# Optimization experiments

Measured on AMD Instinct MI355X. Metric: run time of the kernel, lower is better.

Reference implementation:

```python
import jax, jax.numpy as jnp
import numpy as np
import math

VOCAB, D_MODEL, IN_DIM, OUT_DIM, BLOCK = 50257, 256, 64, 64, 2048

def setup_inputs() -> dict:
    key = jax.random.key(0)
    ks = jax.random.split(key, 8)
    B, S = 4, 1024
    x = jax.random.normal(ks[0], (B, S, IN_DIM), dtype=jnp.float32)
    embedding = jax.random.normal(ks[1], (VOCAB, D_MODEL), dtype=jnp.float32)
    wpe = 0.01 * jax.random.normal(ks[2], (BLOCK, D_MODEL), dtype=jnp.float32)
    lim_e = 1.0 / math.sqrt(IN_DIM)
    enc_w = jax.random.uniform(ks[3], (D_MODEL, IN_DIM), minval=-lim_e, maxval=lim_e, dtype=jnp.float32)
    enc_b = jax.random.uniform(ks[4], (D_MODEL,), minval=-lim_e, maxval=lim_e, dtype=jnp.float32)
    ln_g = jnp.ones((D_MODEL,), dtype=jnp.float32)
    ln_b = jnp.zeros((D_MODEL,), dtype=jnp.float32)
    lim_d = 1.0 / math.sqrt(D_MODEL)
    dec_w = jax.random.uniform(ks[5], (OUT_DIM, D_MODEL), minval=-lim_d, maxval=lim_d, dtype=jnp.float32)
    dec_b = jax.random.uniform(ks[6], (OUT_DIM,), minval=-lim_d, maxval=lim_d, dtype=jnp.float32)
    return {"x": x, "embedding": embedding, "wpe": wpe, "enc_w": enc_w, "enc_b": enc_b,
            "ln_g": ln_g, "ln_b": ln_b, "dec_w": dec_w, "dec_b": dec_b}

def _layernorm(h, g, b, eps=1e-5):
    mu = jnp.mean(h, axis=-1, keepdims=True)
    var = jnp.var(h, axis=-1, keepdims=True)
    return (h - mu) * jax.lax.rsqrt(var + eps) * g + b

def reference(x, embedding, wpe, enc_w, enc_b, ln_g, ln_b, dec_w, dec_b):
    B, S, _ = x.shape
    pos_emb = wpe[:S]                                  # [S, D]
    h = jnp.einsum('bsi,di->bsd', x, enc_w) + enc_b    # encoder
    h = h + pos_emb
    h = _layernorm(h, ln_g, ln_b)
    logits = jnp.einsum('bsd,vd->bsv', h, embedding) / math.sqrt(D_MODEL)
    probs = jax.nn.softmax(logits, axis=-1)            # [B, S, V]
    quantize = jnp.einsum('bsv,vd->bsd', probs, embedding)
    out = jnp.einsum('bsd,od->bso', quantize, dec_w) + dec_b
    return (out, jnp.argmax(probs, axis=-1))
```

## Files before the change

### kernel.cpp

```cpp
#include <hip/hip_runtime.h>
#include <math.h>

#define VOCAB   50257
#define VP      50272
#define NVT     1571
#define DM      256
#define INDIM   64
#define OUTDIM  64
#define NROWS   4096
#define SEQ     1024
#define NSLICE  8
#define NTT     64
#define MARGIN  5e-3f
#define FLAGCAP 1024
#define EP      264
#define FOFF    4.0f

typedef _Float16 f16;
typedef _Float16 half8 __attribute__((ext_vector_type(8)));
typedef _Float16 half4v __attribute__((ext_vector_type(4)));
typedef float floatx4 __attribute__((ext_vector_type(4)));

static __device__ __forceinline__ unsigned ldsaddr(const void* p)
{
    return (unsigned)(unsigned long long)(__attribute__((address_space(3))) const void*)p;
}

template <int NT>
static __device__ __forceinline__ void tr_pair(unsigned a, half4v& t0, half4v& t1)
{
    asm volatile("ds_read_b64_tr_b16 %0, %2 offset:%3\n\t"
                 "ds_read_b64_tr_b16 %1, %2 offset:%4"
                 : "=v"(t0), "=v"(t1)
                 : "v"(a), "i"(NT * 128), "i"(NT * 128 + 2048));
}

__global__ __launch_bounds__(256) void encode_ln_kernel(
    const float* __restrict__ x, const float* __restrict__ enc_w,
    const float* __restrict__ enc_b, const float* __restrict__ wpe,
    const float* __restrict__ ln_g, const float* __restrict__ ln_b,
    float* __restrict__ hs_out, f16* __restrict__ q_hi, f16* __restrict__ q_lo,
    int* flagcnt, int write_q)
{
    const int row = blockIdx.x;
    const int s   = row & (SEQ - 1);
    const int d   = threadIdx.x;

    __shared__ float xs[INDIM];
    __shared__ float w1[4], w2[4];

    if (d < INDIM) xs[d] = x[(size_t)row * INDIM + d];
    __syncthreads();

    const float4* wrow = (const float4*)(enc_w + (size_t)d * INDIM);
    float dot = 0.f;
#pragma unroll
    for (int i = 0; i < INDIM / 4; ++i) {
        float4 w4 = wrow[i];
        dot += w4.x * xs[i * 4 + 0] + w4.y * xs[i * 4 + 1]
             + w4.z * xs[i * 4 + 2] + w4.w * xs[i * 4 + 3];
    }
    float h = dot + enc_b[d] + wpe[(size_t)s * DM + d];

    float v1 = h, v2 = h * h;
#pragma unroll
    for (int mask = 1; mask < 64; mask <<= 1) {
        v1 += __shfl_xor(v1, mask, 64);
        v2 += __shfl_xor(v2, mask, 64);
    }
    if ((d & 63) == 0) { w1[d >> 6] = v1; w2[d >> 6] = v2; }
    __syncthreads();
    float S1 = w1[0] + w1[1] + w1[2] + w1[3];
    float S2 = w2[0] + w2[1] + w2[2] + w2[3];
    float mu  = S1 * (1.f / DM);
    float var = S2 * (1.f / DM) - mu * mu;
    float rs  = rsqrtf(var + 1e-5f);
    float hn  = (h - mu) * rs * ln_g[d] + ln_b[d];
    float hsv = hn * 0.0625f;
    hs_out[(size_t)row * DM + d] = hsv;
    if (write_q) {
        f16 hi = (f16)hsv;
        q_hi[(size_t)row * DM + d] = hi;
        q_lo[(size_t)row * DM + d] = (f16)(hsv - (float)hi);
    }
    if (row == 0 && d == 0 && write_q) *flagcnt = 0;
}

__global__ __launch_bounds__(256) void prep_emb(
    const float* __restrict__ emb, f16* __restrict__ e_hi)
{
    const size_t i = ((size_t)blockIdx.x * 256 + threadIdx.x) * 8;
    if (i >= (size_t)VP * DM) return;
    const size_t v = i >> 8;
    half8 h;
    if (v < VOCAB) {
        const float* src = emb + i;
        float4 f0 = *(const float4*)(src);
        float4 f1 = *(const float4*)(src + 4);
        h[0]=(f16)f0.x; h[1]=(f16)f0.y; h[2]=(f16)f0.z; h[3]=(f16)f0.w;
        h[4]=(f16)f1.x; h[5]=(f16)f1.y; h[6]=(f16)f1.z; h[7]=(f16)f1.w;
    } else {
#pragma unroll
        for (int j = 0; j < 8; ++j) h[j] = (f16)0.f;
    }
    *(half8*)(e_hi + i) = h;
}

__global__ __launch_bounds__(256, 2) void fused_main(
    const f16* __restrict__ e_hi, const f16* __restrict__ q_hi,
    float* __restrict__ pO, float* __restrict__ pm1, float* __restrict__ pm2,
    float* __restrict__ pl, int* __restrict__ pi1)
{
    const int tid  = threadIdx.x;
    const int wave = tid >> 6;
    const int lane = tid & 63;
    const int m_   = lane & 15;
    const int quad = lane >> 4;
    const int slice = blockIdx.x & 7;
    const int tt    = blockIdx.x >> 3;

    __shared__ f16 ehi_s[2][32 * DM];
    __shared__ f16 plds[4][16][40];

    half8 qf[8];
    const f16* qb = q_hi + ((size_t)(tt * 64 + wave * 16 + m_)) * DM + quad * 8;
#pragma unroll
    for (int s = 0; s < 8; ++s) qf[s] = *(const half8*)(qb + s * 32);

    floatx4 O[16];
#pragma unroll
    for (int i = 0; i < 16; ++i) { O[i][0]=0.f; O[i][1]=0.f; O[i][2]=0.f; O[i][3]=0.f; }
    float t1 = -INFINITY, t2 = -INFINITY, lacc = 0.f;
    int   ti = 0;

    const int ntile = (NVT - slice + NSLICE - 1) / NSLICE;

    const int aoff = (m_ >> 2) * 1024 + (m_ & 3) * 16 + (quad >> 1) * 64 + (quad & 1) * 8;

    const unsigned trbase = ldsaddr(&ehi_s[0][0]) + (unsigned)(quad * 4096 + m_ * 2);

    const int ssv = (lane >> 1) & 3;
    const int ssd = ((lane >> 3) << 4) + ((lane & 1) << 3);

#define STAGE_TILE(BB, V0)                                                              \
    {                                                                                   \
        _Pragma("unroll")                                                               \
        for (int i_ = 0; i_ < 2; ++i_) {                                                \
            _Pragma("unroll")                                                           \
            for (int j_ = 0; j_ < 2; ++j_) {                                            \
                const int vblk_ = wave * 2 + i_;                                        \
                const f16* src_ = e_hi + (size_t)((V0) + vblk_ * 4 + ssv) * DM          \
                                  + j_ * 128 + ssd;                                     \
                f16* dst_ = &ehi_s[(BB)][vblk_ * 1024 + j_ * 512];                      \
                __builtin_amdgcn_global_load_lds(                                       \
                    (const __attribute__((address_space(1))) void*)src_,                \
                    (__attribute__((address_space(3))) void*)dst_, 16, 0, 0);           \
            }                                                                           \
        }                                                                               \
    }

    STAGE_TILE(0, slice * 32);
    __syncthreads();

    for (int it = 0; it < ntile; ++it) {
        const int b  = it & 1;
        const int v0 = (slice + it * NSLICE) * 32;
        const bool pre = (it + 1 < ntile);

        if (pre) STAGE_TILE(b ^ 1, v0 + NSLICE * 32);

        floatx4 sf0, sf1;
        sf0[0]=0.f; sf0[1]=0.f; sf0[2]=0.f; sf0[3]=0.f;
        sf1[0]=0.f; sf1[1]=0.f; sf1[2]=0.f; sf1[3]=0.f;
        const f16* ab = &ehi_s[b][aoff];
#pragma unroll
        for (int s = 0; s < 8; ++s) {
            half8 a0 = *(const half8*)(ab + s * 128);
            half8 a1 = *(const half8*)(ab + 4096 + s * 128);
            sf0 = __builtin_amdgcn_mfma_f32_16x16x32_f16(a0, qf[s], sf0, 0, 0, 0);
            sf1 = __builtin_amdgcn_mfma_f32_16x16x32_f16(a1, qf[s], sf1, 0, 0, 0);
        }
        if (v0 + 32 > VOCAB) {
#pragma unroll
            for (int r = 0; r < 4; ++r) {
                if (v0 + quad * 4 + r >= VOCAB)      sf0[r] = -INFINITY;
                if (v0 + 16 + quad * 4 + r >= VOCAB) sf1[r] = -INFINITY;
            }
        }

        float p0[4], p1[4];
#pragma unroll
        for (int r = 0; r < 4; ++r) {
            float sv = sf0[r]; int vg = v0 + quad * 4 + r;
            t2 = fmaxf(t2, fminf(t1, sv));
            ti = (sv > t1) ? vg : ti;
            t1 = fmaxf(t1, sv);
            float e = __expf(sv - FOFF);
            lacc += e; p0[r] = e;
        }
#pragma unroll
        for (int r = 0; r < 4; ++r) {
            float sv = sf1[r]; int vg = v0 + 16 + quad * 4 + r;
            t2 = fmaxf(t2, fminf(t1, sv));
            ti = (sv > t1) ? vg : ti;
            t1 = fmaxf(t1, sv);
            float e = __expf(sv - FOFF);
            lacc += e; p1[r] = e;
        }

        {
            half4v h0, h1;
#pragma unroll
            for (int r = 0; r < 4; ++r) { h0[r] = (f16)p0[r]; h1[r] = (f16)p1[r]; }
            *(half4v*)(&plds[wave][m_][quad * 4])      = h0;
            *(half4v*)(&plds[wave][m_][16 + quad * 4]) = h1;
        }
        __asm__ volatile("s_waitcnt lgkmcnt(0)" ::: "memory");
        half8 a2 = *(const half8*)(&plds[wave][m_][quad * 8]);

        const unsigned trb = trbase + (unsigned)(b * 16384);
        half4v u0[8], u1[8];

        __builtin_amdgcn_sched_barrier(0);
        tr_pair<0>(trb, u0[0], u1[0]);
        tr_pair<1>(trb, u0[1], u1[1]);
        tr_pair<2>(trb, u0[2], u1[2]);
        tr_pair<3>(trb, u0[3], u1[3]);
        tr_pair<4>(trb, u0[4], u1[4]);
        tr_pair<5>(trb, u0[5], u1[5]);
        tr_pair<6>(trb, u0[6], u1[6]);
        tr_pair<7>(trb, u0[7], u1[7]);
        __asm__ volatile("s_waitcnt lgkmcnt(0)" ::: "memory");
        __builtin_amdgcn_sched_barrier(0);
#pragma unroll
        for (int nt = 0; nt < 8; ++nt) {
            half8 b2 = __builtin_shufflevector(u0[nt], u1[nt], 0, 1, 2, 3, 4, 5, 6, 7);
            O[nt] = __builtin_amdgcn_mfma_f32_16x16x32_f16(a2, b2, O[nt], 0, 0, 0);
        }
        tr_pair<8>(trb,  u0[0], u1[0]);
        tr_pair<9>(trb,  u0[1], u1[1]);
        tr_pair<10>(trb, u0[2], u1[2]);
        tr_pair<11>(trb, u0[3], u1[3]);
        tr_pair<12>(trb, u0[4], u1[4]);
        tr_pair<13>(trb, u0[5], u1[5]);
        tr_pair<14>(trb, u0[6], u1[6]);
        tr_pair<15>(trb, u0[7], u1[7]);
        __asm__ volatile("s_waitcnt lgkmcnt(0)" ::: "memory");
        __builtin_amdgcn_sched_barrier(0);
#pragma unroll
        for (int nt = 8; nt < 16; ++nt) {
            half8 b2 = __builtin_shufflevector(u0[nt - 8], u1[nt - 8], 0, 1, 2, 3, 4, 5, 6, 7);
            O[nt] = __builtin_amdgcn_mfma_f32_16x16x32_f16(a2, b2, O[nt], 0, 0, 0);
        }

        __syncthreads();
    }
#undef STAGE_TILE

#pragma unroll
    for (int offc = 16; offc <= 32; offc += 16) {
        float o1 = __shfl_xor(t1, offc);
        float o2 = __shfl_xor(t2, offc);
        int   oi = __shfl_xor(ti, offc);
        float ol = __shfl_xor(lacc, offc);
        t2 = fmaxf(fmaxf(t2, o2), fminf(t1, o1));
        ti = (o1 > t1) ? oi : ti;
        t1 = fmaxf(t1, o1);
        lacc += ol;
    }

    const int trow0 = tt * 64 + wave * 16;
    float* ob = pO + ((size_t)slice * NROWS + trow0) * DM;
#pragma unroll
    for (int nt = 0; nt < 16; ++nt)
#pragma unroll
        for (int r = 0; r < 4; ++r)
            ob[(size_t)(quad * 4 + r) * DM + nt * 16 + m_] = O[nt][r];
    if (lane < 16) {
        const int idx = slice * NROWS + trow0 + lane;
        pm1[idx] = t1;
        pm2[idx] = t2;
        pl [idx] = lacc;
        pi1[idx] = ti;
    }
}

__global__ __launch_bounds__(256) void merge_decode(
    const float* __restrict__ pO, const float* __restrict__ pm1,
    const float* __restrict__ pm2, const float* __restrict__ pl,
    const int* __restrict__ pi1,
    const float* __restrict__ dec_w, const float* __restrict__ dec_b,
    float* __restrict__ out, float* __restrict__ amax_out,
    unsigned long long* __restrict__ amax64, int* flagcnt, int* flaglist,
    int* __restrict__ flbyte)
{
    const int tt  = blockIdx.x;
    const int tid = threadIdx.x;
    __shared__ float q_s[16][DM];
    __shared__ float lI[16];

    if (tid < 16) {
        const int row = tt * 16 + tid;
        float M = -INFINITY, M2 = -INFINITY; int win = 0;
        float lt = 0.f;
        for (int s = 0; s < NSLICE; ++s) {
            float v = pm1[s * NROWS + row];
            if (v > M) { M2 = M; M = v; win = s; }
            else M2 = fmaxf(M2, v);
            M2 = fmaxf(M2, pm2[s * NROWS + row]);
            lt += pl[s * NROWS + row];
        }
        amax_out[row] = (float)pi1[win * NROWS + row];
        amax64[row] = 0ull;
        int fl = (M - M2) < MARGIN;
        flbyte[row] = fl;
        if (fl) {
            int pos = atomicAdd(flagcnt, 1);
            if (pos < FLAGCAP) flaglist[pos] = row;
        }
        lI[tid] = 1.f / lt;
    }
    __syncthreads();
    {
        const int m = tid >> 4, d0 = (tid & 15) * 16;
        const int row = tt * 16 + m;
        float4 acc[4];
#pragma unroll
        for (int k = 0; k < 4; ++k) acc[k] = make_float4(0.f, 0.f, 0.f, 0.f);
        for (int s = 0; s < NSLICE; ++s) {
            const float4* pp = (const float4*)(pO + ((size_t)s * NROWS + row) * DM + d0);
#pragma unroll
            for (int k = 0; k < 4; ++k) {
                float4 v = pp[k];
                acc[k].x += v.x; acc[k].y += v.y;
                acc[k].z += v.z; acc[k].w += v.w;
            }
        }
        const float li = lI[m];
#pragma unroll
        for (int k = 0; k < 4; ++k) {
            acc[k].x *= li; acc[k].y *= li; acc[k].z *= li; acc[k].w *= li;
            *(float4*)&q_s[m][d0 + k * 4] = acc[k];
        }
    }
    __syncthreads();
    {
        const int o = tid & 63;
        const float4* wp = (const float4*)(dec_w + (size_t)o * DM);
#pragma unroll
        for (int k = 0; k < 4; ++k) {
            const int m = (tid >> 6) + k * 4;
            const float4* qp = (const float4*)&q_s[m][0];
            float acc = 0.f;
            for (int d4 = 0; d4 < DM / 4; ++d4) {
                float4 w = wp[d4], q = qp[d4];
                acc += w.x * q.x + w.y * q.y + w.z * q.z + w.w * q.w;
            }
            out[(size_t)(tt * 16 + m) * OUTDIM + o] = acc + dec_b[o];
        }
    }
}

__global__ __launch_bounds__(256) void gather_flagged(
    const f16* __restrict__ q_hi, const f16* __restrict__ q_lo,
    const int* __restrict__ flagcnt, const int* __restrict__ flaglist,
    f16* __restrict__ qg)
{
    int cnt = *flagcnt; if (cnt > FLAGCAP) cnt = FLAGCAP;
    const int j = blockIdx.x;
    if (j >= cnt) return;
    const int row = flaglist[j];
    const int t = threadIdx.x;
    qg[(size_t)j * 512 + t]       = q_hi[(size_t)row * DM + t];
    qg[(size_t)j * 512 + 256 + t] = q_lo[(size_t)row * DM + t];
}

__global__ __launch_bounds__(64) void recheck_rows(
    const float* __restrict__ emb, const f16* __restrict__ qg,
    const int* __restrict__ flagcnt, const int* __restrict__ flaglist,
    unsigned long long* __restrict__ amax64)
{
    int cnt = *flagcnt; if (cnt > FLAGCAP) cnt = FLAGCAP;
    if (cnt == 0) return;
    const int v0   = blockIdx.x * 32;
    const int lane = threadIdx.x;
    const int m_   = lane & 15;
    const int quad = lane >> 4;

    __shared__ f16 ehi[32][EP];
    __shared__ f16 elo[32][EP];

    for (int i = 0; i < 32; ++i) {
        const int v = v0 + i;
        float4 f = (v < VOCAB) ? *(const float4*)(emb + (size_t)v * DM + lane * 4)
                               : make_float4(0.f, 0.f, 0.f, 0.f);
        half4v hh, hl;
        hh[0]=(f16)f.x; hh[1]=(f16)f.y; hh[2]=(f16)f.z; hh[3]=(f16)f.w;
        hl[0]=(f16)(f.x-(float)hh[0]); hl[1]=(f16)(f.y-(float)hh[1]);
        hl[2]=(f16)(f.z-(float)hh[2]); hl[3]=(f16)(f.w-(float)hh[3]);
        *(half4v*)&ehi[i][lane * 4] = hh;
        *(half4v*)&elo[i][lane * 4] = hl;
    }
    __asm__ volatile("s_waitcnt lgkmcnt(0)" ::: "memory");

    for (int c0 = 0; c0 < cnt; c0 += 16) {
        const bool haveb = (c0 + m_) < cnt;
        const int fidx = haveb ? (c0 + m_) : 0;

        half8 bh[8], bl[8];
        const f16* qb = qg + (size_t)fidx * 512 + quad * 8;
#pragma unroll
        for (int s = 0; s < 8; ++s) {
            bh[s] = *(const half8*)(qb + s * 32);
            bl[s] = *(const half8*)(qb + 256 + s * 32);
        }

        floatx4 C0, C1;
        C0[0]=0.f; C0[1]=0.f; C0[2]=0.f; C0[3]=0.f;
        C1[0]=0.f; C1[1]=0.f; C1[2]=0.f; C1[3]=0.f;
#pragma unroll
        for (int s = 0; s < 8; ++s) {
            half8 ah0 = *(const half8*)&ehi[m_][quad * 8 + 32 * s];
            half8 al0 = *(const half8*)&elo[m_][quad * 8 + 32 * s];
            half8 ah1 = *(const half8*)&ehi[m_ + 16][quad * 8 + 32 * s];
            half8 al1 = *(const half8*)&elo[m_ + 16][quad * 8 + 32 * s];
            C0 = __builtin_amdgcn_mfma_f32_16x16x32_f16(ah0, bh[s], C0, 0, 0, 0);
            C0 = __builtin_amdgcn_mfma_f32_16x16x32_f16(ah0, bl[s], C0, 0, 0, 0);
            C0 = __builtin_amdgcn_mfma_f32_16x16x32_f16(al0, bh[s], C0, 0, 0, 0);
            C0 = __builtin_amdgcn_mfma_f32_16x16x32_f16(al0, bl[s], C0, 0, 0, 0);
            C1 = __builtin_amdgcn_mfma_f32_16x16x32_f16(ah1, bh[s], C1, 0, 0, 0);
            C1 = __builtin_amdgcn_mfma_f32_16x16x32_f16(ah1, bl[s], C1, 0, 0, 0);
            C1 = __builtin_amdgcn_mfma_f32_16x16x32_f16(al1, bh[s], C1, 0, 0, 0);
            C1 = __builtin_amdgcn_mfma_f32_16x16x32_f16(al1, bl[s], C1, 0, 0, 0);
        }

        float bv = -INFINITY; int bi = 0;
#pragma unroll
        for (int r = 0; r < 4; ++r) {
            int v = v0 + quad * 4 + r;
            float val = (v < VOCAB) ? C0[r] : -INFINITY;
            if (val > bv) { bv = val; bi = v; }
            int v2 = v + 16;
            float val2 = (v2 < VOCAB) ? C1[r] : -INFINITY;
            if (val2 > bv) { bv = val2; bi = v2; }
        }
#pragma unroll
        for (int offc = 16; offc <= 32; offc += 16) {
            float ov = __shfl_xor(bv, offc);
            int   oi = __shfl_xor(bi, offc);
            if (ov > bv || (ov == bv && oi < bi)) { bv = ov; bi = oi; }
        }
        if (quad == 0 && haveb) {
            unsigned u = __float_as_uint(bv);
            u = (u & 0x80000000u) ? ~u : (u | 0x80000000u);
            unsigned long long key =
                ((unsigned long long)u << 32) | (unsigned)(~bi);
            atomicMax(&amax64[flaglist[fidx]], key);
        }
    }
}

__global__ void finalize_amax(const int* __restrict__ flbyte,
                              const unsigned long long* __restrict__ amax64,
                              float* __restrict__ amax_out)
{
    int row = blockIdx.x * 256 + threadIdx.x;
    if (row >= NROWS) return;
    if (flbyte[row]) {
        unsigned long long u = amax64[row];
        if (u) {
            unsigned idx = ~(unsigned)(u & 0xffffffffu);
            amax_out[row] = (float)idx;
        }
    }
}

#define RPB 4
__global__ __launch_bounds__(256, 2) void fused_softmax_quant_kernel(
    const float* __restrict__ emb, const float* __restrict__ hs,
    const float* __restrict__ dec_w, const float* __restrict__ dec_b,
    float* __restrict__ out, float* __restrict__ amax_out)
{
    const int tid  = threadIdx.x;
    const int g    = tid >> 4;
    const int q    = tid & 15;
    const int row0 = blockIdx.x * RPB;

    __shared__ __align__(16) float q_lds[RPB][DM];
    __shared__ float sm[16][RPB], sl[16][RPB];
    __shared__ int   sam[16][RPB];
    __shared__ float sLf[RPB];

    for (int i = tid; i < RPB * DM; i += 256) (&q_lds[0][0])[i] = 0.f;

    float4 hsr[RPB][4];
#pragma unroll
    for (int r = 0; r < RPB; ++r)
#pragma unroll
        for (int o = 0; o < 4; ++o)
            hsr[r][o] = *(const float4*)(hs + (size_t)(row0 + r) * DM + o * 64 + q * 4);

    float m[RPB], l[RPB];
    int   am[RPB];
    float4 acc[RPB][4];
#pragma unroll
    for (int r = 0; r < RPB; ++r) {
        m[r] = -INFINITY; l[r] = 0.f; am[r] = 0;
#pragma unroll
        for (int o = 0; o < 4; ++o) acc[r][o] = make_float4(0.f, 0.f, 0.f, 0.f);
    }

    float ecur[16], enxt[16];
    {
        size_t b0 = (size_t)g * DM + q * 4;
#pragma unroll
        for (int o = 0; o < 4; ++o)
            *(float4*)(enxt + o * 4) = *(const float4*)(emb + b0 + o * 64);
    }

#pragma unroll 1
    for (int v = g; v < VOCAB; v += 16) {
#pragma unroll
        for (int j = 0; j < 16; ++j) ecur[j] = enxt[j];
        int vn = (v + 16 < VOCAB) ? v + 16 : v;
        size_t bn = (size_t)vn * DM + q * 4;
#pragma unroll
        for (int o = 0; o < 4; ++o)
            *(float4*)(enxt + o * 4) = *(const float4*)(emb + bn + o * 64);

        float part[RPB];
#pragma unroll
        for (int r = 0; r < RPB; ++r) {
            const float* hp = (const float*)&hsr[r][0];
            float t = 0.f;
#pragma unroll
            for (int j = 0; j < 16; ++j) t += ecur[j] * hp[j];
            part[r] = t;
        }
#pragma unroll
        for (int mask = 8; mask >= 1; mask >>= 1)
#pragma unroll
            for (int r = 0; r < RPB; ++r)
                part[r] += __shfl_xor(part[r], mask, 16);

#pragma unroll
        for (int r = 0; r < RPB; ++r) {
            float lg = part[r];
            float* ap = (float*)&acc[r][0];
            if (lg > m[r]) {
                float c = __expf(m[r] - lg);
                m[r] = lg; am[r] = v;
                l[r] = l[r] * c + 1.f;
#pragma unroll
                for (int j = 0; j < 16; ++j) ap[j] = ap[j] * c + ecur[j];
            } else {
                float p = __expf(lg - m[r]);
                l[r] += p;
#pragma unroll
                for (int j = 0; j < 16; ++j) ap[j] += p * ecur[j];
            }
        }
    }

    if (q == 0) {
#pragma unroll
        for (int r = 0; r < RPB; ++r) { sm[g][r] = m[r]; sl[g][r] = l[r]; sam[g][r] = am[r]; }
    }
    __syncthreads();

    float wgt[RPB], Lr[RPB];
    int   A[RPB];
#pragma unroll
    for (int r = 0; r < RPB; ++r) {
        float M = -INFINITY; int a = 0;
        for (int gg = 0; gg < 16; ++gg) {
            float mv = sm[gg][r];
            if (mv > M) { M = mv; a = sam[gg][r]; }
        }
        float L = 0.f;
        for (int gg = 0; gg < 16; ++gg) L += sl[gg][r] * __expf(sm[gg][r] - M);
        wgt[r] = __expf(m[r] - M);
        Lr[r] = L; A[r] = a;
    }

#pragma unroll
    for (int r = 0; r < RPB; ++r) {
        const float* ap = (const float*)&acc[r][0];
#pragma unroll
        for (int j = 0; j < 16; ++j) {
            float vs = ap[j] * wgt[r];
            vs += __shfl_xor(vs, 16, 64);
            vs += __shfl_xor(vs, 32, 64);
            if ((g & 3) == 0) {
                int o = j >> 2, c = j & 3;
                atomicAdd(&q_lds[r][o * 64 + q * 4 + c], vs);
            }
        }
    }
    if (tid == 0) {
#pragma unroll
        for (int r = 0; r < RPB; ++r) {
            sLf[r] = Lr[r];
            amax_out[row0 + r] = (float)A[r];
        }
    }
    __syncthreads();

    {
        const int r = tid >> 6, o = tid & 63;
        const float4* dwp = (const float4*)(dec_w + (size_t)o * DM);
        const float4* qp  = (const float4*)&q_lds[r][0];
        float s = 0.f;
#pragma unroll 8
        for (int d4 = 0; d4 < DM / 4; ++d4) {
            float4 wv = dwp[d4];
            float4 qv = qp[d4];
            s += wv.x * qv.x + wv.y * qv.y + wv.z * qv.z + wv.w * qv.w;
        }
        s = s / sLf[r] + dec_b[o];
        out[(size_t)(row0 + r) * OUTDIM + o] = s;
    }
}

extern "C" void kernel_launch(void* const* d_in, const int* in_sizes, int n_in,
                              void* d_out, int out_size, void* d_ws, size_t ws_size,
                              hipStream_t stream)
{
    const float* x     = (const float*)d_in[0];
    const float* emb   = (const float*)d_in[1];
    const float* wpe   = (const float*)d_in[2];
    const float* enc_w = (const float*)d_in[3];
    const float* enc_b = (const float*)d_in[4];
    const float* ln_g  = (const float*)d_in[5];
    const float* ln_b  = (const float*)d_in[6];
    const float* dec_w = (const float*)d_in[7];
    const float* dec_b = (const float*)d_in[8];

    float* out      = (float*)d_out;
    float* amax_out = out + (size_t)NROWS * OUTDIM;

    char* w = (char*)d_ws;
    size_t off = 0;
    float* hs = (float*)(w + off);          off += (size_t)NROWS * DM * 4;
    f16* q_hi = (f16*)(w + off);            off += (size_t)NROWS * DM * 2;
    f16* q_lo = (f16*)(w + off);            off += (size_t)NROWS * DM * 2;
    f16* e_hi = (f16*)(w + off);            off += (size_t)VP * DM * 2;
    float* pO = (float*)(w + off);          off += (size_t)NSLICE * NROWS * DM * 4;
    float* pm1 = (float*)(w + off);         off += (size_t)NSLICE * NROWS * 4;
    float* pm2 = (float*)(w + off);         off += (size_t)NSLICE * NROWS * 4;
    float* pl  = (float*)(w + off);         off += (size_t)NSLICE * NROWS * 4;
    int*   pi1 = (int*)(w + off);           off += (size_t)NSLICE * NROWS * 4;
    unsigned long long* amax64 = (unsigned long long*)(w + off); off += (size_t)NROWS * 8;
    int* flagcnt  = (int*)(w + off);        off += 256;
    int* flaglist = (int*)(w + off);        off += FLAGCAP * 4;
    int* flbyte   = (int*)(w + off);        off += (size_t)NROWS * 4;
    f16* qg       = (f16*)(w + off);        off += (size_t)FLAGCAP * 512 * 2;

    const bool full = (ws_size >= off);

    encode_ln_kernel<<<NROWS, 256, 0, stream>>>(x, enc_w, enc_b, wpe, ln_g, ln_b,
                                                hs, q_hi, q_lo, flagcnt, full ? 1 : 0);
    if (full) {
        prep_emb<<<((size_t)VP * DM) / (256 * 8), 256, 0, stream>>>(emb, e_hi);
        fused_main<<<NTT * NSLICE, 256, 0, stream>>>(e_hi, q_hi,
                                                     pO, pm1, pm2, pl, pi1);
        merge_decode<<<NROWS / 16, 256, 0, stream>>>(pO, pm1, pm2, pl, pi1, dec_w, dec_b,
                                                     out, amax_out, amax64, flagcnt,
                                                     flaglist, flbyte);
        gather_flagged<<<FLAGCAP, 256, 0, stream>>>(q_hi, q_lo, flagcnt, flaglist, qg);
        recheck_rows<<<NVT, 64, 0, stream>>>(emb, qg, flagcnt, flaglist, amax64);
        finalize_amax<<<(NROWS + 255) / 256, 256, 0, stream>>>(flbyte, amax64, amax_out);
    } else {
        fused_softmax_quant_kernel<<<NROWS / RPB, 256, 0, stream>>>(emb, hs, dec_w,
                                                                    dec_b, out, amax_out);
    }
}
```

Baseline: 545.6 us.

## Switch fused_main to 32x32 MFMA with 64-wide vocab tiles

Rewrites the main logits/softmax/PV kernel to use 32x32x16 MFMA instead of 16x16x32, with 64-vocab tiles per iteration, waves split across token and vocab halves. The prefetch of the next tile moves after a barrier. The per-row max, second max and sum statistics are merged through shared memory at the end. The aim is fewer LDS reads per FLOP and less instruction overhead, at the cost of more LDS, an extra barrier per tile and higher register pressure from four 16-wide accumulators plus 16 q fragments.

```diff
diff --git a/kernel.cpp b/kernel.cpp
--- a/kernel.cpp
+++ b/kernel.cpp
@@ -2,7 +2,8 @@
 #include <math.h>
 
 #define VOCAB   50257
-#define VP      50272
+#define VP64    50304
+#define NT64    786
 #define NVT     1571
 #define DM      256
 #define INDIM   64
@@ -20,19 +21,18 @@
 typedef _Float16 half8 __attribute__((ext_vector_type(8)));
 typedef _Float16 half4v __attribute__((ext_vector_type(4)));
 typedef float floatx4 __attribute__((ext_vector_type(4)));
+typedef float f32x16 __attribute__((ext_vector_type(16)));
 
 static __device__ __forceinline__ unsigned ldsaddr(const void* p)
 {
     return (unsigned)(unsigned long long)(__attribute__((address_space(3))) const void*)p;
 }
 
-template <int NT>
-static __device__ __forceinline__ void tr_pair(unsigned a, half4v& t0, half4v& t1)
-{
-    asm volatile("ds_read_b64_tr_b16 %0, %2 offset:%3\n\t"
-                 "ds_read_b64_tr_b16 %1, %2 offset:%4"
-                 : "=v"(t0), "=v"(t1)
-                 : "v"(a), "i"(NT * 128), "i"(NT * 128 + 2048));
+template <int IMM>
+static __device__ __forceinline__ void trrd(unsigned a, half4v& d)
+{
+    asm volatile("ds_read_b64_tr_b16 %0, %1 offset:%2"
+                 : "=v"(d) : "v"(a), "i"(IMM));
 }
 
 __global__ __launch_bounds__(256) void encode_ln_kernel(
@@ -90,7 +90,7 @@
     const float* __restrict__ emb, f16* __restrict__ e_hi)
 {
     const size_t i = ((size_t)blockIdx.x * 256 + threadIdx.x) * 8;
-    if (i >= (size_t)VP * DM) return;
+    if (i >= (size_t)VP64 * DM) return;
     const size_t v = i >> 8;
     half8 h;
     if (v < VOCAB) {
@@ -114,174 +114,212 @@
     const int tid  = threadIdx.x;
     const int wave = tid >> 6;
     const int lane = tid & 63;
-    const int m_   = lane & 15;
-    const int quad = lane >> 4;
+    const int l31  = lane & 31;
+    const int h    = lane >> 5;
+    const int thalf = wave & 1;
+    const int vhalf = wave >> 1;
     const int slice = blockIdx.x & 7;
     const int tt    = blockIdx.x >> 3;
 
-    __shared__ f16 ehi_s[2][32 * DM];
-    __shared__ f16 plds[4][16][40];
-
-    half8 qf[8];
-    const f16* qb = q_hi + ((size_t)(tt * 64 + wave * 16 + m_)) * DM + quad * 8;
-#pragma unroll
-    for (int s = 0; s < 8; ++s) qf[s] = *(const half8*)(qb + s * 32);
-
-    floatx4 O[16];
-#pragma unroll
-    for (int i = 0; i < 16; ++i) { O[i][0]=0.f; O[i][1]=0.f; O[i][2]=0.f; O[i][3]=0.f; }
-    float t1 = -INFINITY, t2 = -INFINITY, lacc = 0.f;
-    int   ti = 0;
-
-    const int ntile = (NVT - slice + NSLICE - 1) / NSLICE;
-
-    const int aoff = (m_ >> 2) * 1024 + (m_ & 3) * 16 + (quad >> 1) * 64 + (quad & 1) * 8;
-
-    const unsigned trbase = ldsaddr(&ehi_s[0][0]) + (unsigned)(quad * 4096 + m_ * 2);
-
-    const int ssv = (lane >> 1) & 3;
-    const int ssd = ((lane >> 3) << 4) + ((lane & 1) << 3);
-
-#define STAGE_TILE(BB, V0)                                                              \
-    {                                                                                   \
-        _Pragma("unroll")                                                               \
-        for (int i_ = 0; i_ < 2; ++i_) {                                                \
-            _Pragma("unroll")                                                           \
-            for (int j_ = 0; j_ < 2; ++j_) {                                            \
-                const int vblk_ = wave * 2 + i_;                                        \
-                const f16* src_ = e_hi + (size_t)((V0) + vblk_ * 4 + ssv) * DM          \
-                                  + j_ * 128 + ssd;                                     \
-                f16* dst_ = &ehi_s[(BB)][vblk_ * 1024 + j_ * 512];                      \
-                __builtin_amdgcn_global_load_lds(                                       \
-                    (const __attribute__((address_space(1))) void*)src_,                \
-                    (__attribute__((address_space(3))) void*)dst_, 16, 0, 0);           \
-            }                                                                           \
-        }                                                                               \
-    }
-
-    STAGE_TILE(0, slice * 32);
+    __shared__ f16 ehi_s[2][64 * DM];
+    __shared__ f16 plds[64][72];
+    __shared__ float mmrg[2][32][3];
+    __shared__ int   imrg[2][32];
+
+    half8 qf[16];
+    {
+        const f16* qb = q_hi + ((size_t)(tt * 64 + thalf * 32 + l31)) * DM + h * 8;
+#pragma unroll
+        for (int s = 0; s < 16; ++s) qf[s] = *(const half8*)(qb + s * 16);
+    }
+
+    f32x16 O0, O1, O2, O3;
+#pragma unroll
+    for (int i = 0; i < 16; ++i) { O0[i]=0.f; O1[i]=0.f; O2[i]=0.f; O3[i]=0.f; }
+    float t1a = -INFINITY, t2a = -INFINITY, la_a = 0.f;
+    float t1b = -INFINITY, t2b = -INFINITY, la_b = 0.f;
+    int tia = 0, tib = 0;
+
+    const int ntile = (NT64 - slice + NSLICE - 1) / NSLICE;
+
+    const int aoff = (vhalf * 8 + (l31 >> 2)) * 1024 + (l31 & 3) * 16 + h * 8;
+
+    const unsigned trbase = ldsaddr(&ehi_s[0][0]) +
+        (unsigned)(vhalf * 1024 + h * 4096 + ((lane >> 4) & 1) * 128 + (lane & 15) * 2);
+
+    const int lan3 = lane >> 3;
+    const int lv   = (lane & 7) >> 1;
+    const int ld8  = (lane & 1) * 8;
+
+#define STAGE_TILE(BB, V0)                                                   \
+    {                                                                        \
+        _Pragma("unroll")                                                    \
+        for (int c_ = 0; c_ < 8; ++c_) {                                     \
+            const int sub_ = wave * 64 + c_ * 8 + lan3;                      \
+            const int v4_ = sub_ >> 4, d16_ = sub_ & 15;                     \
+            const f16* src_ = e_hi + (size_t)((V0) + v4_ * 4 + lv) * DM      \
+                              + d16_ * 16 + ld8;                             \
+            f16* dst_ = &ehi_s[(BB)][wave * 4096 + c_ * 512];                \
+            __builtin_amdgcn_global_load_lds(                                \
+                (const __attribute__((address_space(1))) void*)src_,         \
+                (__attribute__((address_space(3))) void*)dst_, 16, 0, 0);    \
+        }                                                                    \
+    }
+
+#define G2STEP(DL, OV)                                                         \
+    {                                                                          \
+        half4v u00, u01, u10, u11, u20, u21, u30, u31;                         \
+        trrd<(DL)*256 +     0>(tb, u00);                                       \
+        trrd<(DL)*256 +  2048>(tb, u01);                                       \
+        trrd<(DL)*256 +  8192>(tb, u10);                                       \
+        trrd<(DL)*256 + 10240>(tb, u11);                                       \
+        trrd<(DL)*256 + 16384>(tb, u20);                                       \
+        trrd<(DL)*256 + 18432>(tb, u21);                                       \
+        trrd<(DL)*256 + 24576>(tb, u30);                                       \
+        trrd<(DL)*256 + 26624>(tb, u31);                                       \
+        __asm__ volatile("s_waitcnt lgkmcnt(0)" ::: "memory");                 \
+        __builtin_amdgcn_sched_barrier(0);                                     \
+        __builtin_amdgcn_s_setprio(1);                                         \
+        OV = __builtin_amdgcn_mfma_f32_32x32x16_f16(pa0,                       \
+                 __builtin_shufflevector(u00, u01, 0,1,2,3,4,5,6,7), OV,0,0,0);\
+        OV = __builtin_amdgcn_mfma_f32_32x32x16_f16(pa1,                       \
+                 __builtin_shufflevector(u10, u11, 0,1,2,3,4,5,6,7), OV,0,0,0);\
+        OV = __builtin_amdgcn_mfma_f32_32x32x16_f16(pa2,                       \
+                 __builtin_shufflevector(u20, u21, 0,1,2,3,4,5,6,7), OV,0,0,0);\
+        OV = __builtin_amdgcn_mfma_f32_32x32x16_f16(pa3,                       \
+                 __builtin_shufflevector(u30, u31, 0,1,2,3,4,5,6,7), OV,0,0,0);\
+        __builtin_amdgcn_s_setprio(0);                                         \
+    }
+
+    STAGE_TILE(0, slice * 64);
     __syncthreads();
 
     for (int it = 0; it < ntile; ++it) {
         const int b  = it & 1;
-        const int v0 = (slice + it * NSLICE) * 32;
+        const int v0 = (slice + it * NSLICE) * 64;
         const bool pre = (it + 1 < ntile);
 
-        if (pre) STAGE_TILE(b ^ 1, v0 + NSLICE * 32);
-
-        floatx4 sf0, sf1;
-        sf0[0]=0.f; sf0[1]=0.f; sf0[2]=0.f; sf0[3]=0.f;
-        sf1[0]=0.f; sf1[1]=0.f; sf1[2]=0.f; sf1[3]=0.f;
-        const f16* ab = &ehi_s[b][aoff];
-#pragma unroll
-        for (int s = 0; s < 8; ++s) {
-            half8 a0 = *(const half8*)(ab + s * 128);
-            half8 a1 = *(const half8*)(ab + 4096 + s * 128);
-            sf0 = __builtin_amdgcn_mfma_f32_16x16x32_f16(a0, qf[s], sf0, 0, 0, 0);
-            sf1 = __builtin_amdgcn_mfma_f32_16x16x32_f16(a1, qf[s], sf1, 0, 0, 0);
-        }
-        if (v0 + 32 > VOCAB) {
-#pragma unroll
-            for (int r = 0; r < 4; ++r) {
-                if (v0 + quad * 4 + r >= VOCAB)      sf0[r] = -INFINITY;
-                if (v0 + 16 + quad * 4 + r >= VOCAB) sf1[r] = -INFINITY;
+        f32x16 C;
+#pragma unroll
+        for (int i = 0; i < 16; ++i) C[i] = 0.f;
+        {
+            const f16* ab = &ehi_s[b][aoff];
+            __builtin_amdgcn_s_setprio(1);
+#pragma unroll
+            for (int s = 0; s < 16; ++s)
+                C = __builtin_amdgcn_mfma_f32_32x32x16_f16(
+                        *(const half8*)(ab + s * 64), qf[s], C, 0, 0, 0);
+            __builtin_amdgcn_s_setprio(0);
+        }
+
+        if (v0 + 64 > VOCAB) {
+#pragma unroll
+            for (int r = 0; r < 16; ++r) {
+                int v = v0 + vhalf * 32 + (r & 3) + 8 * (r >> 2) + 4 * h;
+                if (v >= VOCAB) C[r] = -INFINITY;
             }
         }
 
-        float p0[4], p1[4];
-#pragma unroll
-        for (int r = 0; r < 4; ++r) {
-            float sv = sf0[r]; int vg = v0 + quad * 4 + r;
-            t2 = fmaxf(t2, fminf(t1, sv));
-            ti = (sv > t1) ? vg : ti;
-            t1 = fmaxf(t1, sv);
-            float e = __expf(sv - FOFF);
-            lacc += e; p0[r] = e;
-        }
-#pragma unroll
-        for (int r = 0; r < 4; ++r) {
-            float sv = sf1[r]; int vg = v0 + 16 + quad * 4 + r;
-            t2 = fmaxf(t2, fminf(t1, sv));
-            ti = (sv > t1) ? vg : ti;
-            t1 = fmaxf(t1, sv);
-            float e = __expf(sv - FOFF);
-            lacc += e; p1[r] = e;
-        }
-
         {
-            half4v h0, h1;
-#pragma unroll
-            for (int r = 0; r < 4; ++r) { h0[r] = (f16)p0[r]; h1[r] = (f16)p1[r]; }
-            *(half4v*)(&plds[wave][m_][quad * 4])      = h0;
-            *(half4v*)(&plds[wave][m_][16 + quad * 4]) = h1;
-        }
-        __asm__ volatile("s_waitcnt lgkmcnt(0)" ::: "memory");
-        half8 a2 = *(const half8*)(&plds[wave][m_][quad * 8]);
-
-        const unsigned trb = trbase + (unsigned)(b * 16384);
-        half4v u0[8], u1[8];
-
-        __builtin_amdgcn_sched_barrier(0);
-        tr_pair<0>(trb, u0[0], u1[0]);
-        tr_pair<1>(trb, u0[1], u1[1]);
-        tr_pair<2>(trb, u0[2], u1[2]);
-        tr_pair<3>(trb, u0[3], u1[3]);
-        tr_pair<4>(trb, u0[4], u1[4]);
-        tr_pair<5>(trb, u0[5], u1[5]);
-        tr_pair<6>(trb, u0[6], u1[6]);
-        tr_pair<7>(trb, u0[7], u1[7]);
-        __asm__ volatile("s_waitcnt lgkmcnt(0)" ::: "memory");
-        __builtin_amdgcn_sched_barrier(0);
-#pragma unroll
-        for (int nt = 0; nt < 8; ++nt) {
-            half8 b2 = __builtin_shufflevector(u0[nt], u1[nt], 0, 1, 2, 3, 4, 5, 6, 7);
-            O[nt] = __builtin_amdgcn_mfma_f32_16x16x32_f16(a2, b2, O[nt], 0, 0, 0);
-        }
-        tr_pair<8>(trb,  u0[0], u1[0]);
-        tr_pair<9>(trb,  u0[1], u1[1]);
-        tr_pair<10>(trb, u0[2], u1[2]);
-        tr_pair<11>(trb, u0[3], u1[3]);
-        tr_pair<12>(trb, u0[4], u1[4]);
-        tr_pair<13>(trb, u0[5], u1[5]);
-        tr_pair<14>(trb, u0[6], u1[6]);
-        tr_pair<15>(trb, u0[7], u1[7]);
-        __asm__ volatile("s_waitcnt lgkmcnt(0)" ::: "memory");
-        __builtin_amdgcn_sched_barrier(0);
-#pragma unroll
-        for (int nt = 8; nt < 16; ++nt) {
-            half8 b2 = __builtin_shufflevector(u0[nt - 8], u1[nt - 8], 0, 1, 2, 3, 4, 5, 6, 7);
-            O[nt] = __builtin_amdgcn_mfma_f32_16x16x32_f16(a2, b2, O[nt], 0, 0, 0);
+            f16* prow = &plds[thalf * 32 + l31][vhalf * 32 + h * 4];
+#pragma unroll
+            for (int g2 = 0; g2 < 4; ++g2) {
+                half4v hv;
+#pragma unroll
+                for (int j = 0; j < 4; ++j) {
+                    float e = __expf(C[g2 * 4 + j] - FOFF);
+                    hv[j] = (f16)e;
+                    if (g2 < 2) la_a += e; else la_b += e;
+                }
+                *(half4v*)(prow + g2 * 8) = hv;
+            }
+        }
+#pragma unroll
+        for (int r = 0; r < 8; ++r) {
+            float sv = C[r];
+            int vg = v0 + vhalf * 32 + (r & 3) + 8 * (r >> 2) + 4 * h;
+            t2a = fmaxf(t2a, fminf(t1a, sv));
+            tia = (sv > t1a) ? vg : tia;
+            t1a = fmaxf(t1a, sv);
+        }
+#pragma unroll
+        for (int r = 8; r < 16; ++r) {
+            float sv = C[r];
+            int vg = v0 + vhalf * 32 + (r & 3) + 8 * (r >> 2) + 4 * h;
+            t2b = fmaxf(t2b, fminf(t1b, sv));
+            tib = (sv > t1b) ? vg : tib;
+            t1b = fmaxf(t1b, sv);
         }
 
         __syncthreads();
+
+        if (pre) STAGE_TILE(b ^ 1, v0 + NSLICE * 64);
+
+        {
+            const f16* pb = &plds[thalf * 32 + l31][h * 8];
+            half8 pa0 = *(const half8*)(pb);
+            half8 pa1 = *(const half8*)(pb + 16);
+            half8 pa2 = *(const half8*)(pb + 32);
+            half8 pa3 = *(const half8*)(pb + 48);
+            const unsigned tb = trbase + (unsigned)(b * 32768);
+            G2STEP(0, O0)
+            G2STEP(1, O1)
+            G2STEP(2, O2)
+            G2STEP(3, O3)
+        }
+
+        __syncthreads();
     }
 #undef STAGE_TILE
-
-#pragma unroll
-    for (int offc = 16; offc <= 32; offc += 16) {
-        float o1 = __shfl_xor(t1, offc);
-        float o2 = __shfl_xor(t2, offc);
-        int   oi = __shfl_xor(ti, offc);
-        float ol = __shfl_xor(lacc, offc);
-        t2 = fmaxf(fmaxf(t2, o2), fminf(t1, o1));
-        ti = (o1 > t1) ? oi : ti;
-        t1 = fmaxf(t1, o1);
-        lacc += ol;
-    }
-
-    const int trow0 = tt * 64 + wave * 16;
-    float* ob = pO + ((size_t)slice * NROWS + trow0) * DM;
-#pragma unroll
-    for (int nt = 0; nt < 16; ++nt)
-#pragma unroll
-        for (int r = 0; r < 4; ++r)
-            ob[(size_t)(quad * 4 + r) * DM + nt * 16 + m_] = O[nt][r];
-    if (lane < 16) {
-        const int idx = slice * NROWS + trow0 + lane;
-        pm1[idx] = t1;
-        pm2[idx] = t2;
-        pl [idx] = lacc;
-        pi1[idx] = ti;
+#undef G2STEP
+
+    {
+        float* ob = pO + ((size_t)slice * NROWS + tt * 64 + thalf * 32) * DM + vhalf * 128;
+#pragma unroll
+        for (int r = 0; r < 16; ++r) {
+            const size_t rb = (size_t)((r & 3) + 8 * (r >> 2) + 4 * h) * DM + l31;
+            ob[rb +  0] = O0[r];
+            ob[rb + 32] = O1[r];
+            ob[rb + 64] = O2[r];
+            ob[rb + 96] = O3[r];
+        }
+    }
+
+    float nt1 = fmaxf(t1a, t1b);
+    float nt2 = fmaxf(fminf(t1a, t1b), fmaxf(t2a, t2b));
+    int   nti = (t1b > t1a) ? tib : tia;
+    float nl  = la_a + la_b;
+    {
+        float o1 = __shfl_xor(nt1, 32);
+        float o2 = __shfl_xor(nt2, 32);
+        int   oi = __shfl_xor(nti, 32);
+        float ol = __shfl_xor(nl, 32);
+        nt2 = fmaxf(fminf(nt1, o1), fmaxf(nt2, o2));
+        nti = (o1 > nt1) ? oi : nti;
+        nt1 = fmaxf(nt1, o1);
+        nl += ol;
+    }
+    if (vhalf == 1 && h == 0) {
+        mmrg[thalf][l31][0] = nt1;
+        mmrg[thalf][l31][1] = nt2;
+        mmrg[thalf][l31][2] = nl;
+        imrg[thalf][l31] = nti;
+    }
+    __syncthreads();
+    if (vhalf == 0 && h == 0) {
+        float o1 = mmrg[thalf][l31][0];
+        float o2 = mmrg[thalf][l31][1];
+        float ol = mmrg[thalf][l31][2];
+        int   oi = imrg[thalf][l31];
+        nt2 = fmaxf(fminf(nt1, o1), fmaxf(nt2, o2));
+        nti = (o1 > nt1) ? oi : nti;
+        nt1 = fmaxf(nt1, o1);
+        nl += ol;
+        const int idx = slice * NROWS + tt * 64 + thalf * 32 + l31;
+        pm1[idx] = nt1;
+        pm2[idx] = nt2;
+        pl [idx] = nl;
+        pi1[idx] = nti;
     }
 }
 
@@ -644,7 +682,7 @@
     float* hs = (float*)(w + off);          off += (size_t)NROWS * DM * 4;
     f16* q_hi = (f16*)(w + off);            off += (size_t)NROWS * DM * 2;
     f16* q_lo = (f16*)(w + off);            off += (size_t)NROWS * DM * 2;
-    f16* e_hi = (f16*)(w + off);            off += (size_t)VP * DM * 2;
+    f16* e_hi = (f16*)(w + off);            off += (size_t)VP64 * DM * 2;
     float* pO = (float*)(w + off);          off += (size_t)NSLICE * NROWS * DM * 4;
     float* pm1 = (float*)(w + off);         off += (size_t)NSLICE * NROWS * 4;
     float* pm2 = (float*)(w + off);         off += (size_t)NSLICE * NROWS * 4;
@@ -661,7 +699,7 @@
     encode_ln_kernel<<<NROWS, 256, 0, stream>>>(x, enc_w, enc_b, wpe, ln_g, ln_b,
                                                 hs, q_hi, q_lo, flagcnt, full ? 1 : 0);
     if (full) {
-        prep_emb<<<((size_t)VP * DM) / (256 * 8), 256, 0, stream>>>(emb, e_hi);
+        prep_emb<<<((size_t)VP64 * DM) / (256 * 8), 256, 0, stream>>>(emb, e_hi);
         fused_main<<<NTT * NSLICE, 256, 0, stream>>>(e_hi, q_hi,
                                                      pO, pm1, pm2, pl, pi1);
         merge_decode<<<NROWS / 16, 256, 0, stream>>>(pO, pm1, pm2, pl, pi1, dec_w, dec_b,
```

New measurement: 526.1 us. 1.04x faster.
